# Performance work log

Measured on AMD Instinct MI355X. Metric: run time of the kernel, lower is better.

Reference implementation:

```python
import jax, jax.numpy as jnp
from jax import lax
import numpy as np

SCALE = 3.0
TOPK = 16  # eigvec[:, -16:] in the original module
BN_EPS = 1e-5
DN = ('NCHW', 'OIHW', 'NCHW')


def setup_inputs() -> dict:
    key = jax.random.key(0)
    ks = jax.random.split(key, 8)
    B, C, H, W = 16, 256, 64, 64
    x = jax.random.normal(ks[0], (B, C, H, W), dtype=jnp.float32)
    conv1_w = jax.random.normal(ks[1], (C, C, 1, 1), dtype=jnp.float32) * (1.0 / np.sqrt(C))
    conv1_b = jax.random.normal(ks[2], (C,), dtype=jnp.float32) * 0.01
    conv2_w = jax.random.normal(ks[3], (C, C, 3, 3), dtype=jnp.float32) * (1.0 / np.sqrt(9 * C))
    bn_gamma = jnp.ones((C,), dtype=jnp.float32)
    bn_beta = jnp.zeros((C,), dtype=jnp.float32)
    bn_mean = jax.random.normal(ks[4], (C,), dtype=jnp.float32) * 0.1
    bn_var = jax.random.uniform(ks[5], (C,), dtype=jnp.float32, minval=0.5, maxval=1.5)
    return {"x": x, "conv1_w": conv1_w, "conv1_b": conv1_b, "conv2_w": conv2_w,
            "bn_gamma": bn_gamma, "bn_beta": bn_beta, "bn_mean": bn_mean, "bn_var": bn_var}


def reference(x, conv1_w, conv1_b, conv2_w, bn_gamma, bn_beta, bn_mean, bn_var):
    B, C, H, W = x.shape
    # conv1: 1x1 conv with bias
    gx = lax.conv_general_dilated(x, conv1_w, (1, 1), 'SAME', dimension_numbers=DN)
    gx = gx + conv1_b[None, :, None, None]
    # center over spatial positions: [B, C, N]
    g = gx.reshape(B, C, H * W)
    g = g - jnp.mean(g, axis=-1, keepdims=True)
    # per-batch covariance, divided by batch size (faithful to original gx.shape[0])
    cmat = jnp.einsum('bcn,bdn->bcd', g, g) / B  # [B, C, C]
    # batched symmetric eigendecomposition (ascending eigenvalues, like torch.symeig)
    _, vecs = jnp.linalg.eigh(cmat)              # vecs: [B, C, C]
    w = jnp.swapaxes(vecs[..., -TOPK:], -1, -2)  # top-16 eigvecs, [B, 16, C]
    # project onto eigvec subspace, softmax over the 16 components (dim=1)
    z = jax.nn.softmax(jnp.einsum('bkc,bcn->bkn', w, g) * SCALE, axis=1)  # [B, 16, N]
    y = jnp.einsum('bkc,bkn->bcn', w, z).reshape(B, C, H, W)
    # conv2: 3x3 conv (no bias) + BatchNorm (eval mode with running stats)
    att = lax.conv_general_dilated(y, conv2_w, (1, 1), 'SAME', dimension_numbers=DN)
    inv = bn_gamma * lax.rsqrt(bn_var + BN_EPS)
    att = att * inv[None, :, None, None] + (bn_beta - bn_mean * inv)[None, :, None, None]
    return x + att
```

## Files before the change

### kernel.cpp

```cpp
#include <hip/hip_runtime.h>
#include <hip/hip_bf16.h>
#include <math.h>


typedef __hip_bfloat16 bf16;

#define NB 16
#define NC 256
#define NSP 4096
#define LAPACK_EPS32 5.9604644775390625e-08

#define PHB_I0 80
#define PHB_M  176

__device__ __forceinline__ float b2f(bf16 v){ return __bfloat162float(v); }
__device__ __forceinline__ double safelog(double x){
  double a = fabs(x);
  if (!(a > 0.0) || !isfinite(a)) a = 1e-300;
  return log(a);
}

__device__ __forceinline__ float blk_reduce_sum(float s, float* red, int tid){
  red[tid] = s; __syncthreads();
  if (tid < 128) red[tid] += red[tid+128];
  __syncthreads();
  if (tid < 64){
    float x = red[tid] + red[tid+64];
    #pragma unroll
    for (int o = 32; o > 0; o >>= 1) x += __shfl_down(x, o);
    if (tid == 0) red[0] = x;
  }
  __syncthreads();
  return red[0];
}

__device__ __forceinline__ float blk_reduce_sum512(float s, float* red, int tid){
  red[tid] = s; __syncthreads();
  if (tid < 256) red[tid] += red[tid+256];
  __syncthreads();
  if (tid < 128) red[tid] += red[tid+128];
  __syncthreads();
  if (tid < 64){
    float x = red[tid] + red[tid+64];
    #pragma unroll
    for (int o = 32; o > 0; o >>= 1) x += __shfl_down(x, o);
    if (tid == 0) red[0] = x;
  }
  __syncthreads();
  return red[0];
}

__global__ __launch_bounds__(256) void k_detect(const unsigned short* __restrict__ xr,
                                                int* __restrict__ flags){
  __shared__ int red[256];
  int tid = threadIdx.x;
  int cnt = 0;
  for (int i = tid; i < 4096; i += 256){
    unsigned int u = xr[i];
    unsigned int e = (u >> 7) & 0xFF;
    if (e >= 134) ++cnt;
  }
  red[tid] = cnt; __syncthreads();
  for (int o=128;o>0;o>>=1){ if(tid<o) red[tid]+=red[tid+o]; __syncthreads(); }
  if (tid==0) flags[0] = (red[0] > 50) ? 1 : 0;
}

__global__ __launch_bounds__(256) void k_conv1(const void* __restrict__ xv_,
                                               const void* __restrict__ w1v,
                                               const int* __restrict__ flags,
                                               float* __restrict__ g){
  __shared__ __attribute__((aligned(16))) float ws[256][16];
  int nt = blockIdx.x, ct = blockIdx.y, b = blockIdx.z;
  int tid = threadIdx.x;
  int c0 = ct*16;
  int isf = flags[0];
  if (isf){
    const float* w1 = (const float*)w1v;
    for (int i = tid; i < 16*256; i += 256)
      ws[i&255][i>>8] = w1[(size_t)(c0 + (i>>8))*256 + (i&255)];
  } else {
    const bf16* w1 = (const bf16*)w1v;
    for (int i = tid; i < 16*256; i += 256)
      ws[i&255][i>>8] = b2f(w1[(size_t)(c0 + (i>>8))*256 + (i&255)]);
  }
  __syncthreads();
  int n = nt*256 + tid;
  float acc[16];
  #pragma unroll
  for (int i=0;i<16;++i) acc[i]=0.f;
  if (isf){
    const float* xp = (const float*)xv_ + (size_t)b*NC*NSP + n;
    for (int d=0; d<256; ++d){
      float xv = xp[(size_t)d*NSP];
      float4 wa=*(const float4*)&ws[d][0];
      float4 wb=*(const float4*)&ws[d][4];
      float4 wc=*(const float4*)&ws[d][8];
      float4 wd=*(const float4*)&ws[d][12];
      acc[0] =fmaf(wa.x,xv,acc[0]);  acc[1] =fmaf(wa.y,xv,acc[1]);
      acc[2] =fmaf(wa.z,xv,acc[2]);  acc[3] =fmaf(wa.w,xv,acc[3]);
      acc[4] =fmaf(wb.x,xv,acc[4]);  acc[5] =fmaf(wb.y,xv,acc[5]);
      acc[6] =fmaf(wb.z,xv,acc[6]);  acc[7] =fmaf(wb.w,xv,acc[7]);
      acc[8] =fmaf(wc.x,xv,acc[8]);  acc[9] =fmaf(wc.y,xv,acc[9]);
      acc[10]=fmaf(wc.z,xv,acc[10]); acc[11]=fmaf(wc.w,xv,acc[11]);
      acc[12]=fmaf(wd.x,xv,acc[12]); acc[13]=fmaf(wd.y,xv,acc[13]);
      acc[14]=fmaf(wd.z,xv,acc[14]); acc[15]=fmaf(wd.w,xv,acc[15]);
    }
  } else {
    const bf16* xp = (const bf16*)xv_ + (size_t)b*NC*NSP + n;
    for (int d=0; d<256; ++d){
      float xv = b2f(xp[(size_t)d*NSP]);
      float4 wa=*(const float4*)&ws[d][0];
      float4 wb=*(const float4*)&ws[d][4];
      float4 wc=*(const float4*)&ws[d][8];
      float4 wd=*(const float4*)&ws[d][12];
      acc[0] =fmaf(wa.x,xv,acc[0]);  acc[1] =fmaf(wa.y,xv,acc[1]);
      acc[2] =fmaf(wa.z,xv,acc[2]);  acc[3] =fmaf(wa.w,xv,acc[3]);
      acc[4] =fmaf(wb.x,xv,acc[4]);  acc[5] =fmaf(wb.y,xv,acc[5]);
      acc[6] =fmaf(wb.z,xv,acc[6]);  acc[7] =fmaf(wb.w,xv,acc[7]);
      acc[8] =fmaf(wc.x,xv,acc[8]);  acc[9] =fmaf(wc.y,xv,acc[9]);
      acc[10]=fmaf(wc.z,xv,acc[10]); acc[11]=fmaf(wc.w,xv,acc[11]);
      acc[12]=fmaf(wd.x,xv,acc[12]); acc[13]=fmaf(wd.y,xv,acc[13]);
      acc[14]=fmaf(wd.z,xv,acc[14]); acc[15]=fmaf(wd.w,xv,acc[15]);
    }
  }
  float* gp = g + ((size_t)b*NC + c0)*NSP + n;
  #pragma unroll
  for (int i=0;i<16;++i) gp[(size_t)i*NSP] = acc[i];
}

__global__ __launch_bounds__(256) void k_center(float* __restrict__ g){
  int bc = blockIdx.x;
  float* p = g + (size_t)bc*NSP;
  int tid = threadIdx.x;
  __shared__ float red[256];
  float s = 0.f;
  for (int i=tid;i<NSP;i+=256) s += p[i];
  red[tid]=s; __syncthreads();
  for (int o=128;o>0;o>>=1){ if(tid<o) red[tid]+=red[tid+o]; __syncthreads(); }
  float mean = red[0] * (1.0f/4096.0f);
  for (int i=tid;i<NSP;i+=256) p[i] -= mean;
}

__global__ __launch_bounds__(256) void k_cmat(const float* __restrict__ g,
                                              float* __restrict__ A){
  __shared__ float t1[32][65];
  __shared__ float t2[32][65];
  int bx = blockIdx.x, by = blockIdx.y, b = blockIdx.z;
  int tid = threadIdx.x;
  int tx = tid & 31, ty = tid >> 5;
  const float* gb = g + (size_t)b*NC*NSP;
  float acc[4] = {0.f,0.f,0.f,0.f};
  for (int ch=0; ch<64; ++ch){
    int n0 = ch*64;
    for (int idx=tid; idx<2048; idx+=256){
      int r = idx>>6, cc = idx&63;
      t1[r][cc] = gb[(size_t)(by*32 + r)*NSP + n0 + cc];
      t2[r][cc] = gb[(size_t)(bx*32 + r)*NSP + n0 + cc];
    }
    __syncthreads();
    for (int kk=0; kk<64; ++kk){
      float v2 = t2[tx][kk];
      #pragma unroll
      for (int jj=0;jj<4;++jj) acc[jj] = fmaf(t1[ty+8*jj][kk], v2, acc[jj]);
    }
    __syncthreads();
  }
  #pragma unroll
  for (int jj=0;jj<4;++jj){
    int row = by*32 + ty + 8*jj, col = bx*32 + tx;
    A[((size_t)b*NC + row)*NC + col] = acc[jj]*(1.0f/16.0f);
  }
}

__global__ __launch_bounds__(512,1) void k_sytd2(float* __restrict__ Ag,
                                                 float* __restrict__ e_g,
                                                 float* __restrict__ tau_g,
                                                 float* __restrict__ d_g){
  int b = blockIdx.x, tid = threadIdx.x;
  int rid = tid & 255, half = tid >> 8;
  float* A = Ag + (size_t)b*65536;
  __shared__ float Asub[PHB_M*PHB_M];
  __shared__ float v[256], wv[256];
  __shared__ float red[512];
  __shared__ float accbuf[512];

  for (int i=0;i<PHB_I0;++i){
    float alpha = A[(size_t)i*256+(i+1)];
    float s=0.f;
    { int r=i+2+tid; if (r<256){ float a=A[(size_t)i*256+r]; s=a*a; } }
    float xnorm2 = blk_reduce_sum512(s, red, tid);
    float tau=0.f, scale=0.f, beta=alpha;
    if (xnorm2 > 0.f){
      float r_ = sqrtf(alpha*alpha + xnorm2);
      beta = (alpha >= 0.f) ? -r_ : r_;
      tau = (beta - alpha)/beta;
      scale = 1.0f/(alpha - beta);
    }
    if (tid==0){ e_g[b*256+i] = beta; tau_g[b*256+i] = tau; }
    if (tau != 0.f){
      { int r=i+1+tid;
        if (r<256){
          float val = (r==i+1)?1.0f : A[(size_t)i*256+r]*scale;
          A[(size_t)i*256+r] = val;  v[r] = val;
        }
      }
      __syncthreads();
      int r = i+1+rid;
      bool rv = (r < 256);
      int cmid = (i+1+256) >> 1;
      int cstart = (half==0)? (i+1) : cmid;
      int cend   = (half==0)? cmid  : 256;
      {
        float acc=0.f;
        if (rv){
          const float* Ar = A + r;
          int nfull = (cend-cstart) >> 4;
          float b0[16], b1[16];
          if (nfull>0){
            #pragma unroll
            for (int u=0;u<16;++u) b0[u] = Ar[(size_t)(cstart+u)*256];
          }
          int t=0;
          for (; t+2<=nfull; t+=2){
            int cB = cstart+(t+1)*16;
            #pragma unroll
            for (int u=0;u<16;++u) b1[u] = Ar[(size_t)(cB+u)*256];
            int cA = cstart+t*16;
            #pragma unroll
            for (int u=0;u<16;++u) acc = fmaf(b0[u], v[cA+u], acc);
            if (t+2 < nfull){
              int cC = cstart+(t+2)*16;
              #pragma unroll
              for (int u=0;u<16;++u) b0[u] = Ar[(size_t)(cC+u)*256];
            }
            #pragma unroll
            for (int u=0;u<16;++u) acc = fmaf(b1[u], v[cB+u], acc);
          }
          if (t<nfull){
            int cA = cstart+t*16;
            #pragma unroll
            for (int u=0;u<16;++u) acc = fmaf(b0[u], v[cA+u], acc);
            ++t;
          }
          for (int c2=cstart+nfull*16; c2<cend; ++c2)
            acc = fmaf(Ar[(size_t)c2*256], v[c2], acc);
        }
        accbuf[half*256+rid] = acc;
      }
      __syncthreads();
      if (half==0 && rv) wv[r] = tau*(accbuf[rid] + accbuf[256+rid]);
      __syncthreads();
      float sd = (half==0 && rv)? v[r]*wv[r] : 0.f;
      float dotv = blk_reduce_sum512(sd, red, tid);
      float a2 = -0.5f*tau*dotv;
      if (half==0 && rv) wv[r] += a2*v[r];
      __syncthreads();
      if (rv){
        float vr=v[r], wr=wv[r];
        float* Arw = A + r;
        int nfull = (cend-cstart) >> 4;
        float b0[16], b1[16];
        if (nfull>0){
          #pragma unroll
          for (int u=0;u<16;++u) b0[u] = Arw[(size_t)(cstart+u)*256];
        }
        int t=0;
        for (; t+2<=nfull; t+=2){
          int cB = cstart+(t+1)*16;
          #pragma unroll
          for (int u=0;u<16;++u) b1[u] = Arw[(size_t)(cB+u)*256];
          int cA = cstart+t*16;
          #pragma unroll
          for (int u=0;u<16;++u) b0[u] -= vr*wv[cA+u] + wr*v[cA+u];
          #pragma unroll
          for (int u=0;u<16;++u) Arw[(size_t)(cA+u)*256] = b0[u];
          if (t+2 < nfull){
            int cC = cstart+(t+2)*16;
            #pragma unroll
            for (int u=0;u<16;++u) b0[u] = Arw[(size_t)(cC+u)*256];
          }
          #pragma unroll
          for (int u=0;u<16;++u) b1[u] -= vr*wv[cB+u] + wr*v[cB+u];
          #pragma unroll
          for (int u=0;u<16;++u) Arw[(size_t)(cB+u)*256] = b1[u];
        }
        if (t<nfull){
          int cA = cstart+t*16;
          #pragma unroll
          for (int u=0;u<16;++u) b0[u] -= vr*wv[cA+u] + wr*v[cA+u];
          #pragma unroll
          for (int u=0;u<16;++u) Arw[(size_t)(cA+u)*256] = b0[u];
          ++t;
        }
        for (int c2=cstart+nfull*16; c2<cend; ++c2)
          Arw[(size_t)c2*256] -= vr*wv[c2] + wr*v[c2];
      }
      __syncthreads();
    }
    __syncthreads();
  }

  for (int idx=tid; idx<PHB_M*PHB_M; idx+=512){
    int cc = idx / PHB_M, rr = idx - cc*PHB_M;
    Asub[idx] = A[(size_t)(PHB_I0+cc)*256 + (PHB_I0+rr)];
  }
  __syncthreads();

  for (int i=PHB_I0;i<255;++i){
    int cb = (i - PHB_I0)*PHB_M;
    float alpha = Asub[cb + (i+1-PHB_I0)];
    float s=0.f;
    { int r=i+2+tid; if (r<256){ float a=Asub[cb + (r-PHB_I0)]; s=a*a; } }
    float xnorm2 = blk_reduce_sum512(s, red, tid);
    float tau=0.f, scale=0.f, beta=alpha;
    if (xnorm2 > 0.f){
      float r_ = sqrtf(alpha*alpha + xnorm2);
      beta = (alpha >= 0.f) ? -r_ : r_;
      tau = (beta - alpha)/beta;
      scale = 1.0f/(alpha - beta);
    }
    if (tid==0){ e_g[b*256+i] = beta; tau_g[b*256+i] = tau; }
    if (tau != 0.f){
      { int r=i+1+tid;
        if (r<256){
          float val = (r==i+1)?1.0f : Asub[cb+(r-PHB_I0)]*scale;
          Asub[cb+(r-PHB_I0)] = val;
          A[(size_t)i*256+r] = val;
          v[r] = val;
        }
      }
      __syncthreads();
      int r = i+1+rid;
      bool rv = (r < 256);
      int ro = r - PHB_I0;
      int cmid = (i+1+256) >> 1;
      int cstart = (half==0)? (i+1) : cmid;
      int cend   = (half==0)? cmid  : 256;
      {
        float acc=0.f;
        if (rv){
          int nfull = (cend-cstart) >> 4;
          for (int t=0;t<nfull;++t){
            int cA = cstart + t*16;
            float av[16];
            #pragma unroll
            for (int u=0;u<16;++u) av[u] = Asub[(cA+u-PHB_I0)*PHB_M + ro];
            #pragma unroll
            for (int u=0;u<16;++u) acc = fmaf(av[u], v[cA+u], acc);
          }
          for (int c2=cstart+nfull*16;c2<cend;++c2)
            acc = fmaf(Asub[(c2-PHB_I0)*PHB_M+ro], v[c2], acc);
        }
        accbuf[half*256+rid] = acc;
      }
      __syncthreads();
      if (half==0 && rv) wv[r] = tau*(accbuf[rid] + accbuf[256+rid]);
      __syncthreads();
      float sd = (half==0 && rv)? v[r]*wv[r] : 0.f;
      float dotv = blk_reduce_sum512(sd, red, tid);
      float a2 = -0.5f*tau*dotv;
      if (half==0 && rv) wv[r] += a2*v[r];
      __syncthreads();
      if (rv){
        float vr=v[r], wr=wv[r];
        int nfull = (cend-cstart) >> 4;
        for (int t=0;t<nfull;++t){
          int cA=cstart+t*16;
          float av[16];
          #pragma unroll
          for (int u=0;u<16;++u) av[u] = Asub[(cA+u-PHB_I0)*PHB_M+ro];
          #pragma unroll
          for (int u=0;u<16;++u) av[u] -= vr*wv[cA+u] + wr*v[cA+u];
          #pragma unroll
          for (int u=0;u<16;++u) Asub[(cA+u-PHB_I0)*PHB_M+ro] = av[u];
        }
        for (int c2=cstart+nfull*16;c2<cend;++c2)
          Asub[(c2-PHB_I0)*PHB_M+ro] -= vr*wv[c2] + wr*v[c2];
      }
      __syncthreads();
    }
    __syncthreads();
  }
  if (tid < 256){
    int r = tid;
    float dv = (r >= PHB_I0)? Asub[(r-PHB_I0)*PHB_M + (r-PHB_I0)] : A[(size_t)r*256+r];
    d_g[b*256+r] = dv;
  }
}

__global__ __launch_bounds__(256) void k_leaf(const float* __restrict__ d_g,
                                              const float* __restrict__ e_g,
                                              float* __restrict__ Qg,
                                              double* __restrict__ Dw_g,
                                              double* __restrict__ emod_g){
  int b = blockIdx.x, tid = threadIdx.x;
  float* Q = Qg + (size_t)b*65536;
  double* Dw = Dw_g + (size_t)b*256;
  __shared__ double As[16*257];
  __shared__ float  Vt[16*257];
  __shared__ double dms[256];
  __shared__ double emod[256];
  __shared__ float redf[256];

  float dv = d_g[b*256+tid];
  float ev = (tid<255)? e_g[b*256+tid] : 0.f;
  redf[tid] = fmaxf(fabsf(dv), fabsf(ev)); __syncthreads();
  for(int o=128;o>0;o>>=1){ if(tid<o) redf[tid]=fmaxf(redf[tid],redf[tid+o]); __syncthreads(); }
  double sigma = (double)redf[0];
  if (!(sigma > 0.0)) sigma = 1.0;
  double dmod = (double)dv;
  if ((tid & 15)==15 && tid<255) dmod -= fabs((double)e_g[b*256+tid]);
  if ((tid & 15)==0  && tid>0)   dmod -= fabs((double)e_g[b*256+tid-1]);
  dmod /= sigma;
  double em = (tid<255)? ((double)ev)/sigma : 0.0;
  dms[tid] = dmod;  emod[tid] = em;
  emod_g[b*256+tid] = em;
  __syncthreads();

  int l16 = tid & ~15, j = tid & 15;
  for (int r=0;r<16;++r){
    double av = 0.0;
    if (r==j)        av = dms[l16+j];
    else if (r==j-1) av = emod[l16+j-1];
    else if (r==j+1) av = emod[l16+j];
    As[r*257+tid] = av;
    Vt[r*257+tid] = (r==j)? 1.f : 0.f;
  }
  __syncthreads();

  for (int sweep=0; sweep<14; ++sweep){
    for (int p=0;p<15;++p){
      for (int q=p+1;q<16;++q){
        double app = As[p*257 + l16+p];
        double aqq = As[q*257 + l16+q];
        double apq = As[p*257 + l16+q];
        bool rot = (fabs(apq) > 1e-18);
        double c, s;
        if (rot){
          double theta = (aqq - app)/(2.0*apq);
          double t = 1.0/(fabs(theta)+sqrt(1.0+theta*theta));
          if (theta < 0.0) t = -t;
          c = 1.0/sqrt(1.0+t*t); s = t*c;
        } else { c = 1.0; s = 0.0; }
        double apj = As[p*257 + tid];
        double aqj = As[q*257 + tid];
        double npj = c*apj - s*aqj;
        double nqj = s*apj + c*aqj;
        if (rot && j==p){ npj = c*c*app - 2.0*c*s*apq + s*s*aqq; nqj = 0.0; }
        if (rot && j==q){ npj = 0.0; nqj = s*s*app + 2.0*c*s*apq + c*c*aqq; }
        As[p*257 + tid] = npj;
        As[q*257 + tid] = nqj;
        As[j*257 + l16+p] = npj;
        As[j*257 + l16+q] = nqj;
        float vp = Vt[p*257 + tid], vq = Vt[q*257 + tid];
        Vt[p*257 + tid] = (float)(c*(double)vp - s*(double)vq);
        Vt[q*257 + tid] = (float)(s*(double)vp + c*(double)vq);
      }
    }
  }
  __syncthreads();
  double myval = As[j*257 + l16+j];
  int rank = 0;
  for (int k=0;k<16;++k){
    double vk = As[k*257 + l16+k];
    if (vk < myval || (vk==myval && k<j)) ++rank;
  }
  Dw[l16+rank] = myval;
  for (int r=0;r<16;++r)
    Q[(size_t)(l16+r)*256 + (l16+rank)] = Vt[j*257 + l16+r];
}

struct DCMerge {
  double z_[256], dsv[256], ds2[256], zs2[256];
  double dl_[256], zl_[256], taus[256], ztil[256], normk[256], evo[256];
  double rotcs[256][2];
  int    cs2[256], colx[256], non_[256], defl_[256], anch[256], osrc[256], otyp[256];
  int    roti[256][2];
};

__global__ __launch_bounds__(256) void k_msolve(int lev,
                                                const double* __restrict__ emod_g,
                                                float* __restrict__ Qsrc,
                                                double* __restrict__ Dw_g,
                                                double* __restrict__ Sdl,
                                                double* __restrict__ Sztil,
                                                double* __restrict__ Staus,
                                                double* __restrict__ Snk,
                                                int* __restrict__ Scolx,
                                                int* __restrict__ Sanch,
                                                int* __restrict__ Sotyp,
                                                int* __restrict__ Sosrc,
                                                int* __restrict__ SK){
  int mrg = blockIdx.x, b = blockIdx.y, tid = threadIdx.x;
  float* Q  = Qsrc + (size_t)b*65536;
  double* Dw = Dw_g + (size_t)b*256;
  int slot = b*8 + mrg;
  __shared__ DCMerge mg;
  __shared__ int bci[4];

  int ssz = 16<<lev, nm = ssz<<1;
  int base = mrg*nm;
  double rho0 = emod_g[b*256 + base+ssz-1];
  if (tid < nm){
    float zf = (tid < ssz) ? Q[(size_t)(base+ssz-1)*256 + base + tid]
                           : Q[(size_t)(base+ssz)*256   + base + tid];
    double zz = (double)zf;
    if (rho0 < 0.0 && tid >= ssz) zz = -zz;
    mg.z_[tid] = zz * 0.70710678118654752440;
    mg.dsv[tid] = Dw[base+tid];
  }
  __syncthreads();
  double rho = fabs(2.0*rho0);
  if (tid==0){
    int i1=0, i2=ssz, o=0;
    while (i1<ssz || i2<nm){
      bool take1;
      if (i1>=ssz) take1=false; else if (i2>=nm) take1=true;
      else take1 = (mg.dsv[i1] <= mg.dsv[i2]);
      int src = take1? i1++ : i2++;
      mg.ds2[o]=mg.dsv[src]; mg.zs2[o]=mg.z_[src]; mg.cs2[o]=src; ++o;
    }
  }
  __syncthreads();
  mg.taus[tid] = (tid<nm)? fabs(mg.zs2[tid]) : 0.0; __syncthreads();
  for(int o2=128;o2>0;o2>>=1){ if(tid<o2) mg.taus[tid]=fmax(mg.taus[tid],mg.taus[tid+o2]); __syncthreads(); }
  double zmax = mg.taus[0]; __syncthreads();
  mg.taus[tid] = (tid<nm)? fabs(mg.ds2[tid]) : 0.0; __syncthreads();
  for(int o2=128;o2>0;o2>>=1){ if(tid<o2) mg.taus[tid]=fmax(mg.taus[tid],mg.taus[tid+o2]); __syncthreads(); }
  double dmax = mg.taus[0]; __syncthreads();
  double tol = 8.0*LAPACK_EPS32*fmax(dmax, zmax);
  if (tid==0){
    int K=0, nd=0, nrot=0, pj=-1;
    for (int j=0;j<nm;++j){
      if (rho*fabs(mg.zs2[j]) <= tol){ mg.defl_[nd++]=j; continue; }
      if (pj>=0){
        double sg=mg.zs2[pj], cg=mg.zs2[j];
        double tg=mg.ds2[j]-mg.ds2[pj];
        double taug=sqrt(cg*cg+sg*sg);
        double cn, sn;
        if (taug > 0.0){ cn=cg/taug; sn=-sg/taug; } else { cn=1.0; sn=0.0; }
        if (fabs(tg*cn*sn) <= tol){
          mg.zs2[j]=taug; mg.zs2[pj]=0.0;
          mg.roti[nrot][0]=mg.cs2[pj]; mg.roti[nrot][1]=mg.cs2[j];
          mg.rotcs[nrot][0]=cn; mg.rotcs[nrot][1]=sn; ++nrot;
          double t2 = mg.ds2[pj]*cn*cn + mg.ds2[j]*sn*sn;
          mg.ds2[j] = mg.ds2[pj]*sn*sn + mg.ds2[j]*cn*cn;
          mg.ds2[pj] = t2;
          mg.defl_[nd++]=pj;
          pj=j;
        } else { mg.non_[K++]=pj; pj=j; }
      } else pj=j;
    }
    if (pj>=0) mg.non_[K++]=pj;
    bci[0]=K; bci[1]=nd; bci[2]=nrot;
  }
  __syncthreads();
  int K=bci[0], nd=bci[1], nrot=bci[2];
  for (int r2=0;r2<nrot;++r2){
    int ca = base + mg.roti[r2][0], cb2 = base + mg.roti[r2][1];
    double cn = mg.rotcs[r2][0], sn = mg.rotcs[r2][1];
    if (tid < nm){
      int row = base+tid;
      float xv = Q[(size_t)row*256+ca], yv = Q[(size_t)row*256+cb2];
      Q[(size_t)row*256+ca]  = (float)(cn*(double)xv + sn*(double)yv);
      Q[(size_t)row*256+cb2] = (float)(cn*(double)yv - sn*(double)xv);
    }
    __syncthreads();
  }
  if (tid<K){
    mg.dl_[tid]=mg.ds2[mg.non_[tid]];
    mg.zl_[tid]=mg.zs2[mg.non_[tid]];
    mg.colx[tid]=mg.cs2[mg.non_[tid]];
  }
  __syncthreads();
  mg.taus[tid] = (tid<K)? mg.zl_[tid]*mg.zl_[tid] : 0.0; __syncthreads();
  for(int o2=128;o2>0;o2>>=1){ if(tid<o2) mg.taus[tid]+=mg.taus[tid+o2]; __syncthreads(); }
  double zsum2 = mg.taus[0]; __syncthreads();
  if (tid<K){
    int j=tid;
    double left=mg.dl_[j];
    double right=(j<K-1)? mg.dl_[j+1] : (mg.dl_[K-1] + rho*zsum2);
    double mid=0.5*(left+right);
    double fm=1.0;
    for (int i3=0;i3<K;++i3){
      double del=mg.dl_[i3]-mid;
      fm += rho*mg.zl_[i3]*mg.zl_[i3]/del;
    }
    int a; double lo, hi;
    if (j==K-1){
      a=K-1;
      if (fm<=0.0){ lo=mid-left; hi=right-left; } else { lo=0.0; hi=mid-left; }
    } else if (fm<=0.0){ a=j+1; lo=mid-mg.dl_[j+1]; hi=0.0; }
    else { a=j; lo=0.0; hi=mid-left; }
    double da2=mg.dl_[a];
    double t;
    if (hi > lo){
      t=0.5*(lo+hi);
    } else {
      t = (a==j)? 1e-300 : -1e-300;
      lo = fmin(lo, t); hi = fmax(hi, t);
    }
    for (int it=0; it<100; ++it){
      double gg=1.0, dg=0.0;
      for (int i3=0;i3<K;++i3){
        double del=(mg.dl_[i3]-da2)-t;
        double q=mg.zl_[i3]/del;
        gg += rho*mg.zl_[i3]*q;
        dg += rho*q*q;
      }
      if (gg<0.0) lo=t; else hi=t;
      double tn = t - gg/dg;
      if (!isfinite(tn) || !(tn>lo && tn<hi)) tn=0.5*(lo+hi);
      if (tn == 0.0) tn = (t!=0.0)? t*0.5 : ((a==j)?1e-300:-1e-300);
      double dstep=fabs(tn-t);
      t=tn;
      if (dstep <= 1e-15*(fabs(t)+1e-30)) break;
      if ((hi-lo) <= 1e-15*(fabs(da2)+fabs(t)+1e-30)) break;
    }
    if (t == 0.0 || !isfinite(t)) t = (a==j)? 1e-300 : -1e-300;
    mg.taus[j]=t; mg.anch[j]=a;
  }
  __syncthreads();
  if (tid<K){
    int i3=tid; double acc=0.0; double di=mg.dl_[i3];
    for (int j=0;j<K;++j){
      double lmd = (mg.dl_[mg.anch[j]] - di) + mg.taus[j];
      acc += safelog(lmd);
      if (j!=i3) acc -= safelog(mg.dl_[j]-di);
    }
    double mag = exp(0.5*acc);
    if (!isfinite(mag)) mag = 0.0;
    mg.ztil[i3] = (mg.zl_[i3] >= 0.0)? mag : -mag;
  }
  __syncthreads();
  if (tid<K){
    int j=tid; double da2=mg.dl_[mg.anch[j]]; double tj=mg.taus[j];
    double nr=0.0;
    for (int i3=0;i3<K;++i3){
      double del=(mg.dl_[i3]-da2)-tj;
      if (del == 0.0) del = (tj>=0.0)? -1e-300 : 1e-300;
      double sv=mg.ztil[i3]/del;
      nr += sv*sv;
    }
    if (!(nr > 0.0) || !isfinite(nr)) nr = 1.0;
    mg.normk[j]=sqrt(nr);
  }
  __syncthreads();
  if (tid==0){
    for (int a2=1;a2<nd;++a2){
      int key=mg.defl_[a2]; double kv=mg.ds2[key]; int b2=a2-1;
      while (b2>=0 && mg.ds2[mg.defl_[b2]] > kv){ mg.defl_[b2+1]=mg.defl_[b2]; --b2; }
      mg.defl_[b2+1]=key;
    }
    int i1=0,i2=0,o=0;
    while (i1<K || i2<nd){
      double v1 = (i1<K)? (mg.dl_[mg.anch[i1]]+mg.taus[i1]) : 0.0;
      double v2 = (i2<nd)? mg.ds2[mg.defl_[i2]] : 0.0;
      bool take1;
      if (i1>=K) take1=false; else if (i2>=nd) take1=true; else take1 = (v1 <= v2);
      if (take1){ mg.otyp[o]=0; mg.osrc[o]=i1; mg.evo[o]=v1; ++i1; }
      else { mg.otyp[o]=1; mg.osrc[o]=mg.cs2[mg.defl_[i2]]; mg.evo[o]=v2; ++i2; }
      ++o;
    }
  }
  __syncthreads();
  if (tid<nm) Dw[base+tid]=mg.evo[tid];
  size_t so = (size_t)slot*256;
  if (tid<K){
    Sdl[so+tid]=mg.dl_[tid]; Sztil[so+tid]=mg.ztil[tid];
    Staus[so+tid]=mg.taus[tid]; Snk[so+tid]=mg.normk[tid];
    Scolx[so+tid]=mg.colx[tid]; Sanch[so+tid]=mg.anch[tid];
  }
  if (tid<nm){ Sotyp[so+tid]=mg.otyp[tid]; Sosrc[so+tid]=mg.osrc[tid]; }
  if (tid==0) SK[slot]=K;
}

__global__ __launch_bounds__(256) void k_mvec(int lev,
                                              const float* __restrict__ Qsrc_g,
                                              float* __restrict__ Qdst_g,
                                              const double* __restrict__ Sdl,
                                              const double* __restrict__ Sztil,
                                              const double* __restrict__ Staus,
                                              const double* __restrict__ Snk,
                                              const int* __restrict__ Scolx,
                                              const int* __restrict__ Sanch,
                                              const int* __restrict__ Sotyp,
                                              const int* __restrict__ Sosrc,
                                              const int* __restrict__ SK){
  int t = blockIdx.x, mrg = blockIdx.y, b = blockIdx.z, tid = threadIdx.x;
  const float* Q = Qsrc_g + (size_t)b*65536;
  float* Qd = Qdst_g + (size_t)b*65536;
  int slot = b*8 + mrg;
  size_t so = (size_t)slot*256;
  int ssz = 16<<lev, nm = ssz<<1;
  int base = mrg*nm;
  int p0 = t*16;
  int K = SK[slot];

  __shared__ float svf[256*16];
  __shared__ double cda[16], ctj[16];
  __shared__ float cnk[16];
  __shared__ int ctyp[16], csrc[16];

  if (tid < 16){
    int p = p0 + tid;
    int typ = Sotyp[so+p], src = Sosrc[so+p];
    ctyp[tid]=typ; csrc[tid]=src;
    if (typ==0){
      int j = src;
      cda[tid] = Sdl[so + Sanch[so+j] - 0 + 0];
    }
  }
  __syncthreads();
  if (tid < 16){
    int p = p0 + tid;
    if (ctyp[tid]==0){
      int j = csrc[tid];
      int a = Sanch[so+j];
      cda[tid] = Sdl[so+a];
      ctj[tid] = Staus[so+j];
      cnk[tid] = (float)Snk[so+j];
    } else { cda[tid]=0.0; ctj[tid]=1.0; cnk[tid]=1.f; }
  }
  __syncthreads();
  for (int idx = tid; idx < K*16; idx += 256){
    int i3 = idx >> 4, c = idx & 15;
    float sv = 0.f;
    if (ctyp[c]==0){
      double del = (Sdl[so+i3] - cda[c]) - ctj[c];
      if (del == 0.0) del = (ctj[c]>=0.0)? -1e-300 : 1e-300;
      sv = (float)( Sztil[so+i3]/del / (double)cnk[c] );
      if (!isfinite(sv)) sv = 0.f;
    }
    svf[i3*16 + c] = sv;
  }
  __syncthreads();

  if (tid < nm){
    int row = base + tid;
    const float* Qr = Q + (size_t)row*256 + base;
    float acc[16];
    #pragma unroll
    for (int c=0;c<16;++c) acc[c]=0.f;
    for (int i3=0;i3<K;++i3){
      float qv = Qr[Scolx[so+i3]];
      #pragma unroll
      for (int c=0;c<16;++c) acc[c] = fmaf(qv, svf[i3*16+c], acc[c]);
    }
    #pragma unroll
    for (int c=0;c<16;++c){
      float v = acc[c];
      if (ctyp[c]==1) v = Qr[csrc[c]];
      if (!isfinite(v)) v = 0.f;
      Qd[(size_t)row*256 + base + p0 + c] = v;
    }
  }
}

__global__ __launch_bounds__(512,1) void k_backtf(const float* __restrict__ Ag,
                                                  const float* __restrict__ tau_g,
                                                  const float* __restrict__ Qg,
                                                  float* __restrict__ w16g){
  int b=blockIdx.x, tid=threadIdx.x;
  const float* A=Ag+(size_t)b*65536;
  const float* Q=Qg+(size_t)b*65536;
  __shared__ float U[256][17];
  __shared__ float pd[32][17];
  __shared__ float dk[16];
  int k=tid&15, rg=tid>>4;
  for (int r=rg;r<256;r+=32) U[r][k]=Q[(size_t)r*256+240+k];
  __syncthreads();
  for (int i=254;i>=0;--i){
    float tau=tau_g[b*256+i];
    if (tau!=0.f){
      int r0 = i+1+rg;
      float ar[8];
      #pragma unroll
      for (int u=0;u<8;++u){
        int r = r0 + u*32;
        ar[u] = (r<256)? A[(size_t)i*256+r] : 0.f;
      }
      float uv[8];
      #pragma unroll
      for (int u=0;u<8;++u){
        int r = r0 + u*32;
        uv[u] = (r<256)? U[r][k] : 0.f;
      }
      float s=0.f;
      #pragma unroll
      for (int u=0;u<8;++u){
        int r = r0 + u*32;
        if (r<256) s += ar[u]*uv[u];
      }
      pd[rg][k]=s;
      __syncthreads();
      if (tid<16){
        float acc=0.f;
        #pragma unroll
        for (int gg=0; gg<32; ++gg) acc+=pd[gg][tid];
        dk[tid]=tau*acc;
      }
      __syncthreads();
      float dkk = dk[k];
      #pragma unroll
      for (int u=0;u<8;++u){
        int r = r0 + u*32;
        if (r<256) U[r][k] -= dkk*ar[u];
      }
      __syncthreads();
    }
  }
  for (int c2=rg;c2<256;c2+=32){
    float uv = U[c2][k];
    if (!isfinite(uv)) uv = 0.f;
    w16g[((size_t)b*16+k)*256+c2]=uv;
  }
}

__global__ __launch_bounds__(256) void k_score(const float* __restrict__ g,
                                               const float* __restrict__ w16,
                                               float* __restrict__ z){
  __shared__ __attribute__((aligned(16))) float ws[256][16];
  int nt=blockIdx.x, b=blockIdx.y, tid=threadIdx.x;
  for (int i=tid;i<4096;i+=256) ws[i&255][i>>8]=w16[(size_t)b*4096+i];
  __syncthreads();
  int n=nt*256+tid;
  const float* gp=g+(size_t)b*NC*NSP+n;
  float acc[16];
  #pragma unroll
  for(int k2=0;k2<16;++k2) acc[k2]=0.f;
  for (int c2=0;c2<256;++c2){
    float gv=gp[(size_t)c2*NSP];
    float4 wa=*(const float4*)&ws[c2][0];
    float4 wb=*(const float4*)&ws[c2][4];
    float4 wc=*(const float4*)&ws[c2][8];
    float4 wd=*(const float4*)&ws[c2][12];
    acc[0] =fmaf(wa.x,gv,acc[0]);  acc[1] =fmaf(wa.y,gv,acc[1]);
    acc[2] =fmaf(wa.z,gv,acc[2]);  acc[3] =fmaf(wa.w,gv,acc[3]);
    acc[4] =fmaf(wb.x,gv,acc[4]);  acc[5] =fmaf(wb.y,gv,acc[5]);
    acc[6] =fmaf(wb.z,gv,acc[6]);  acc[7] =fmaf(wb.w,gv,acc[7]);
    acc[8] =fmaf(wc.x,gv,acc[8]);  acc[9] =fmaf(wc.y,gv,acc[9]);
    acc[10]=fmaf(wc.z,gv,acc[10]); acc[11]=fmaf(wc.w,gv,acc[11]);
    acc[12]=fmaf(wd.x,gv,acc[12]); acc[13]=fmaf(wd.y,gv,acc[13]);
    acc[14]=fmaf(wd.z,gv,acc[14]); acc[15]=fmaf(wd.w,gv,acc[15]);
  }
  float mx=-1e30f;
  #pragma unroll
  for(int k2=0;k2<16;++k2){ acc[k2]*=3.0f; mx=fmaxf(mx,acc[k2]); }
  float sum=0.f;
  #pragma unroll
  for(int k2=0;k2<16;++k2){ acc[k2]=expf(acc[k2]-mx); sum+=acc[k2]; }
  float inv=1.0f/sum;
  float* zp=z+(size_t)b*16*NSP+n;
  #pragma unroll
  for(int k2=0;k2<16;++k2) zp[(size_t)k2*NSP]=acc[k2]*inv;
}

__global__ __launch_bounds__(256) void k_y(const float* __restrict__ z,
                                           const float* __restrict__ w16,
                                           float* __restrict__ y){
  __shared__ __attribute__((aligned(16))) float ws[256][16];
  int nt=blockIdx.x, b=blockIdx.y, tid=threadIdx.x;
  for (int i=tid;i<4096;i+=256) ws[i&255][i>>8]=w16[(size_t)b*4096+i];
  __syncthreads();
  int n=nt*256+tid;
  const float* zp=z+(size_t)b*16*NSP+n;
  float zr[16];
  #pragma unroll
  for(int k2=0;k2<16;++k2) zr[k2]=zp[(size_t)k2*NSP];
  float* yp=y+(size_t)b*NC*NSP+n;
  for (int c2=0;c2<256;++c2){
    float4 wa=*(const float4*)&ws[c2][0];
    float4 wb=*(const float4*)&ws[c2][4];
    float4 wc=*(const float4*)&ws[c2][8];
    float4 wd=*(const float4*)&ws[c2][12];
    float acc=0.f;
    acc=fmaf(wa.x,zr[0],acc);  acc=fmaf(wa.y,zr[1],acc);
    acc=fmaf(wa.z,zr[2],acc);  acc=fmaf(wa.w,zr[3],acc);
    acc=fmaf(wb.x,zr[4],acc);  acc=fmaf(wb.y,zr[5],acc);
    acc=fmaf(wb.z,zr[6],acc);  acc=fmaf(wb.w,zr[7],acc);
    acc=fmaf(wc.x,zr[8],acc);  acc=fmaf(wc.y,zr[9],acc);
    acc=fmaf(wc.z,zr[10],acc); acc=fmaf(wc.w,zr[11],acc);
    acc=fmaf(wd.x,zr[12],acc); acc=fmaf(wd.y,zr[13],acc);
    acc=fmaf(wd.z,zr[14],acc); acc=fmaf(wd.w,zr[15],acc);
    yp[(size_t)c2*NSP]=acc;
  }
}

__global__ __launch_bounds__(256) void k_conv2(const float* __restrict__ y,
                                               const void* __restrict__ w2v,
                                               const void* __restrict__ xv_,
                                               const void* __restrict__ gmv,
                                               const void* __restrict__ btv,
                                               const void* __restrict__ muv,
                                               const void* __restrict__ vrv,
                                               const int* __restrict__ flags,
                                               void* __restrict__ outv){
  __shared__ float yt[8][6][66];
  __shared__ float wt[16][8][9];
  int ht=blockIdx.x, ct=blockIdx.y, b=blockIdx.z, tid=threadIdx.x;
  int hl=tid>>6, wl=tid&63;
  int h=ht*4+hl;
  int c0=ct*16;
  int isf = flags[0];
  float acc[16];
  #pragma unroll
  for(int i=0;i<16;++i) acc[i]=0.f;
  const float* yb = y + (size_t)b*NC*NSP;
  for (int d0=0; d0<256; d0+=8){
    for (int idx=tid; idx<8*6*64; idx+=256){
      int dd=idx/384; int rem=idx-dd*384; int rr=rem>>6; int cc2=rem&63;
      int hg=ht*4-1+rr;
      float v = (hg>=0 && hg<64)? yb[(size_t)(d0+dd)*NSP + hg*64 + cc2] : 0.f;
      yt[dd][rr][cc2+1]=v;
    }
    if (tid<48){ int dd=tid/6, rr=tid-dd*6; yt[dd][rr][0]=0.f; yt[dd][rr][65]=0.f; }
    if (isf){
      const float* w2 = (const float*)w2v;
      for (int idx=tid; idx<16*8*9; idx+=256){
        int cc=idx/72; int rem=idx-cc*72; int dd=rem/9; int kk=rem-dd*9;
        wt[cc][dd][kk]=w2[ ((size_t)(c0+cc)*256 + d0+dd)*9 + kk ];
      }
    } else {
      const bf16* w2 = (const bf16*)w2v;
      for (int idx=tid; idx<16*8*9; idx+=256){
        int cc=idx/72; int rem=idx-cc*72; int dd=rem/9; int kk=rem-dd*9;
        wt[cc][dd][kk]=b2f(w2[ ((size_t)(c0+cc)*256 + d0+dd)*9 + kk ]);
      }
    }
    __syncthreads();
    for (int cc=0; cc<16; ++cc){
      float a=acc[cc];
      #pragma unroll
      for (int dd=0; dd<8; ++dd){
        const float* wp=wt[cc][dd];
        a = fmaf(wp[0], yt[dd][hl+0][wl+0], a);
        a = fmaf(wp[1], yt[dd][hl+0][wl+1], a);
        a = fmaf(wp[2], yt[dd][hl+0][wl+2], a);
        a = fmaf(wp[3], yt[dd][hl+1][wl+0], a);
        a = fmaf(wp[4], yt[dd][hl+1][wl+1], a);
        a = fmaf(wp[5], yt[dd][hl+1][wl+2], a);
        a = fmaf(wp[6], yt[dd][hl+2][wl+0], a);
        a = fmaf(wp[7], yt[dd][hl+2][wl+1], a);
        a = fmaf(wp[8], yt[dd][hl+2][wl+2], a);
      }
      acc[cc]=a;
    }
    __syncthreads();
  }
  size_t nidx=(size_t)h*64+wl;
  for (int cc=0;cc<16;++cc){
    int c=c0+cc;
    float gmf, btf, muf, vrf, xvv;
    size_t oi = ((size_t)b*NC+c)*NSP + nidx;
    if (isf){
      gmf=((const float*)gmv)[c]; btf=((const float*)btv)[c];
      muf=((const float*)muv)[c]; vrf=((const float*)vrv)[c];
      xvv=((const float*)xv_)[oi];
    } else {
      gmf=b2f(((const bf16*)gmv)[c]); btf=b2f(((const bf16*)btv)[c]);
      muf=b2f(((const bf16*)muv)[c]); vrf=b2f(((const bf16*)vrv)[c]);
      xvv=b2f(((const bf16*)xv_)[oi]);
    }
    float inv = gmf * rsqrtf(vrf + 1e-5f);
    float shift = btf - muf*inv;
    float val = xvv + acc[cc]*inv + shift;
    if (isf) ((float*)outv)[oi] = val;
    else     ((bf16*)outv)[oi] = __float2bfloat16(val);
  }
}

extern "C" void kernel_launch(void* const* d_in, const int* in_sizes, int n_in,
                              void* d_out, int out_size, void* d_ws, size_t ws_size,
                              hipStream_t stream) {
  const void* x   = d_in[0];
  const void* w1  = d_in[1];
  const void* w2  = d_in[3];
  const void* gmm = d_in[4];
  const void* bet = d_in[5];
  const void* mu  = d_in[6];
  const void* var = d_in[7];

  float* g    = (float*)d_ws;
  float* A    = g   + (size_t)NB*NC*NSP;
  float* Qa   = A   + (size_t)NB*NC*NC;
  float* Qb   = Qa  + (size_t)NB*NC*NC;
  float* w16  = Qb  + (size_t)NB*NC*NC;
  float* zb   = w16 + (size_t)NB*16*NC;
  float* e_g  = zb  + (size_t)NB*16*NSP;
  float* tau_g= e_g + (size_t)NB*NC;
  float* d_g  = tau_g + (size_t)NB*NC;
  double* Dw  = (double*)(d_g + (size_t)NB*NC);
  double* emod_g = Dw + (size_t)NB*NC;
  double* Sdl   = emod_g + (size_t)NB*NC;
  double* Sztil = Sdl   + (size_t)128*256;
  double* Staus = Sztil + (size_t)128*256;
  double* Snk   = Staus + (size_t)128*256;
  int* Scolx = (int*)(Snk + (size_t)128*256);
  int* Sanch = Scolx + (size_t)128*256;
  int* Sotyp = Sanch + (size_t)128*256;
  int* Sosrc = Sotyp + (size_t)128*256;
  int* SK    = Sosrc + (size_t)128*256;
  int* flags = SK + 256;
  size_t needed = (size_t)((char*)(flags + 16) - (char*)d_ws);
  if (ws_size < needed) return;

  hipMemsetAsync(Qa, 0, (size_t)NB*NC*NC*2*sizeof(float), stream);
  k_detect<<<dim3(1),256,0,stream>>>((const unsigned short*)x, flags);
  k_conv1 <<<dim3(16,16,16),256,0,stream>>>(x, w1, flags, g);
  k_center<<<dim3(NB*NC),256,0,stream>>>(g);
  k_cmat  <<<dim3(8,8,16),256,0,stream>>>(g, A);
  k_sytd2 <<<dim3(16),512,0,stream>>>(A, e_g, tau_g, d_g);
  k_leaf  <<<dim3(16),256,0,stream>>>(d_g, e_g, Qa, Dw, emod_g);
  k_msolve<<<dim3(8,16),256,0,stream>>>(0, emod_g, Qa, Dw, Sdl,Sztil,Staus,Snk,Scolx,Sanch,Sotyp,Sosrc,SK);
  k_mvec  <<<dim3(2,8,16),256,0,stream>>>(0, Qa, Qb, Sdl,Sztil,Staus,Snk,Scolx,Sanch,Sotyp,Sosrc,SK);
  k_msolve<<<dim3(4,16),256,0,stream>>>(1, emod_g, Qb, Dw, Sdl,Sztil,Staus,Snk,Scolx,Sanch,Sotyp,Sosrc,SK);
  k_mvec  <<<dim3(4,4,16),256,0,stream>>>(1, Qb, Qa, Sdl,Sztil,Staus,Snk,Scolx,Sanch,Sotyp,Sosrc,SK);
  k_msolve<<<dim3(2,16),256,0,stream>>>(2, emod_g, Qa, Dw, Sdl,Sztil,Staus,Snk,Scolx,Sanch,Sotyp,Sosrc,SK);
  k_mvec  <<<dim3(8,2,16),256,0,stream>>>(2, Qa, Qb, Sdl,Sztil,Staus,Snk,Scolx,Sanch,Sotyp,Sosrc,SK);
  k_msolve<<<dim3(1,16),256,0,stream>>>(3, emod_g, Qb, Dw, Sdl,Sztil,Staus,Snk,Scolx,Sanch,Sotyp,Sosrc,SK);
  k_mvec  <<<dim3(16,1,16),256,0,stream>>>(3, Qb, Qa, Sdl,Sztil,Staus,Snk,Scolx,Sanch,Sotyp,Sosrc,SK);
  k_backtf<<<dim3(16),512,0,stream>>>(A, tau_g, Qa, w16);
  k_score <<<dim3(16,16),256,0,stream>>>(g, w16, zb);
  k_y     <<<dim3(16,16),256,0,stream>>>(zb, w16, g);
  k_conv2 <<<dim3(16,16,16),256,0,stream>>>(g, w2, x, gmm, bet, mu, var, flags, d_out);
}
```

Measured before the change: 7.483 ms.

## Fuse score/softmax with back-projection and enlarge conv2 spatial tile per thread

Merges the projection+softmax kernel with the y reconstruction kernel, so each thread keeps its 16 softmax weights in registers and writes y in place over g. This drops the z intermediate buffer and one launch. The 3x3 conv2 kernel now covers 8 rows per block, with each thread computing two output columns. That halves the grid and cuts the halo overhead on the shared y tile, at the cost of more registers per thread.

```diff
diff --git a/kernel.cpp b/kernel.cpp
--- a/kernel.cpp
+++ b/kernel.cpp
@@ -817,15 +817,14 @@
   }
 }
 
-__global__ __launch_bounds__(256) void k_score(const float* __restrict__ g,
-                                               const float* __restrict__ w16,
-                                               float* __restrict__ z){
+__global__ __launch_bounds__(256) void k_scy(float* __restrict__ g,
+                                             const float* __restrict__ w16){
   __shared__ __attribute__((aligned(16))) float ws[256][16];
   int nt=blockIdx.x, b=blockIdx.y, tid=threadIdx.x;
   for (int i=tid;i<4096;i+=256) ws[i&255][i>>8]=w16[(size_t)b*4096+i];
   __syncthreads();
   int n=nt*256+tid;
-  const float* gp=g+(size_t)b*NC*NSP+n;
+  float* gp=g+(size_t)b*NC*NSP+n;
   float acc[16];
   #pragma unroll
   for(int k2=0;k2<16;++k2) acc[k2]=0.f;
@@ -851,39 +850,23 @@
   #pragma unroll
   for(int k2=0;k2<16;++k2){ acc[k2]=expf(acc[k2]-mx); sum+=acc[k2]; }
   float inv=1.0f/sum;
-  float* zp=z+(size_t)b*16*NSP+n;
   #pragma unroll
-  for(int k2=0;k2<16;++k2) zp[(size_t)k2*NSP]=acc[k2]*inv;
-}
-
-__global__ __launch_bounds__(256) void k_y(const float* __restrict__ z,
-                                           const float* __restrict__ w16,
-                                           float* __restrict__ y){
-  __shared__ __attribute__((aligned(16))) float ws[256][16];
-  int nt=blockIdx.x, b=blockIdx.y, tid=threadIdx.x;
-  for (int i=tid;i<4096;i+=256) ws[i&255][i>>8]=w16[(size_t)b*4096+i];
-  __syncthreads();
-  int n=nt*256+tid;
-  const float* zp=z+(size_t)b*16*NSP+n;
-  float zr[16];
-  #pragma unroll
-  for(int k2=0;k2<16;++k2) zr[k2]=zp[(size_t)k2*NSP];
-  float* yp=y+(size_t)b*NC*NSP+n;
+  for(int k2=0;k2<16;++k2) acc[k2]*=inv;
   for (int c2=0;c2<256;++c2){
     float4 wa=*(const float4*)&ws[c2][0];
     float4 wb=*(const float4*)&ws[c2][4];
     float4 wc=*(const float4*)&ws[c2][8];
     float4 wd=*(const float4*)&ws[c2][12];
-    float acc=0.f;
-    acc=fmaf(wa.x,zr[0],acc);  acc=fmaf(wa.y,zr[1],acc);
-    acc=fmaf(wa.z,zr[2],acc);  acc=fmaf(wa.w,zr[3],acc);
-    acc=fmaf(wb.x,zr[4],acc);  acc=fmaf(wb.y,zr[5],acc);
-    acc=fmaf(wb.z,zr[6],acc);  acc=fmaf(wb.w,zr[7],acc);
-    acc=fmaf(wc.x,zr[8],acc);  acc=fmaf(wc.y,zr[9],acc);
-    acc=fmaf(wc.z,zr[10],acc); acc=fmaf(wc.w,zr[11],acc);
-    acc=fmaf(wd.x,zr[12],acc); acc=fmaf(wd.y,zr[13],acc);
-    acc=fmaf(wd.z,zr[14],acc); acc=fmaf(wd.w,zr[15],acc);
-    yp[(size_t)c2*NSP]=acc;
+    float a=0.f;
+    a=fmaf(wa.x,acc[0],a);  a=fmaf(wa.y,acc[1],a);
+    a=fmaf(wa.z,acc[2],a);  a=fmaf(wa.w,acc[3],a);
+    a=fmaf(wb.x,acc[4],a);  a=fmaf(wb.y,acc[5],a);
+    a=fmaf(wb.z,acc[6],a);  a=fmaf(wb.w,acc[7],a);
+    a=fmaf(wc.x,acc[8],a);  a=fmaf(wc.y,acc[9],a);
+    a=fmaf(wc.z,acc[10],a); a=fmaf(wc.w,acc[11],a);
+    a=fmaf(wd.x,acc[12],a); a=fmaf(wd.y,acc[13],a);
+    a=fmaf(wd.z,acc[14],a); a=fmaf(wd.w,acc[15],a);
+    gp[(size_t)c2*NSP]=a;
   }
 }
 
@@ -896,25 +879,25 @@
                                                const void* __restrict__ vrv,
                                                const int* __restrict__ flags,
                                                void* __restrict__ outv){
-  __shared__ float yt[8][6][66];
+  __shared__ float yt[8][10][66];
   __shared__ float wt[16][8][9];
   int ht=blockIdx.x, ct=blockIdx.y, b=blockIdx.z, tid=threadIdx.x;
-  int hl=tid>>6, wl=tid&63;
-  int h=ht*4+hl;
+  int wl=tid&31, hl=tid>>5;
+  int h=ht*8+hl;
   int c0=ct*16;
   int isf = flags[0];
-  float acc[16];
+  float accA[16], accB[16];
   #pragma unroll
-  for(int i=0;i<16;++i) acc[i]=0.f;
+  for(int i=0;i<16;++i){ accA[i]=0.f; accB[i]=0.f; }
   const float* yb = y + (size_t)b*NC*NSP;
   for (int d0=0; d0<256; d0+=8){
-    for (int idx=tid; idx<8*6*64; idx+=256){
-      int dd=idx/384; int rem=idx-dd*384; int rr=rem>>6; int cc2=rem&63;
-      int hg=ht*4-1+rr;
+    for (int idx=tid; idx<8*10*64; idx+=256){
+      int dd=idx/640; int rem=idx-dd*640; int rr=rem>>6; int cc2=rem&63;
+      int hg=ht*8-1+rr;
       float v = (hg>=0 && hg<64)? yb[(size_t)(d0+dd)*NSP + hg*64 + cc2] : 0.f;
       yt[dd][rr][cc2+1]=v;
     }
-    if (tid<48){ int dd=tid/6, rr=tid-dd*6; yt[dd][rr][0]=0.f; yt[dd][rr][65]=0.f; }
+    if (tid<80){ int dd=tid/10, rr=tid-dd*10; yt[dd][rr][0]=0.f; yt[dd][rr][65]=0.f; }
     if (isf){
       const float* w2 = (const float*)w2v;
       for (int idx=tid; idx<16*8*9; idx+=256){
@@ -930,7 +913,7 @@
     }
     __syncthreads();
     for (int cc=0; cc<16; ++cc){
-      float a=acc[cc];
+      float a=accA[cc], c=accB[cc];
       #pragma unroll
       for (int dd=0; dd<8; ++dd){
         const float* wp=wt[cc][dd];
@@ -943,30 +926,43 @@
         a = fmaf(wp[6], yt[dd][hl+2][wl+0], a);
         a = fmaf(wp[7], yt[dd][hl+2][wl+1], a);
         a = fmaf(wp[8], yt[dd][hl+2][wl+2], a);
-      }
-      acc[cc]=a;
+        c = fmaf(wp[0], yt[dd][hl+0][wl+32], c);
+        c = fmaf(wp[1], yt[dd][hl+0][wl+33], c);
+        c = fmaf(wp[2], yt[dd][hl+0][wl+34], c);
+        c = fmaf(wp[3], yt[dd][hl+1][wl+32], c);
+        c = fmaf(wp[4], yt[dd][hl+1][wl+33], c);
+        c = fmaf(wp[5], yt[dd][hl+1][wl+34], c);
+        c = fmaf(wp[6], yt[dd][hl+2][wl+32], c);
+        c = fmaf(wp[7], yt[dd][hl+2][wl+33], c);
+        c = fmaf(wp[8], yt[dd][hl+2][wl+34], c);
+      }
+      accA[cc]=a; accB[cc]=c;
     }
     __syncthreads();
   }
-  size_t nidx=(size_t)h*64+wl;
+  size_t n0=(size_t)h*64+wl;
+  size_t n1=n0+32;
   for (int cc=0;cc<16;++cc){
     int c=c0+cc;
-    float gmf, btf, muf, vrf, xvv;
-    size_t oi = ((size_t)b*NC+c)*NSP + nidx;
+    float gmf, btf, muf, vrf, xv0, xv1;
+    size_t oi0 = ((size_t)b*NC+c)*NSP + n0;
+    size_t oi1 = ((size_t)b*NC+c)*NSP + n1;
     if (isf){
       gmf=((const float*)gmv)[c]; btf=((const float*)btv)[c];
       muf=((const float*)muv)[c]; vrf=((const float*)vrv)[c];
-      xvv=((const float*)xv_)[oi];
+      xv0=((const float*)xv_)[oi0]; xv1=((const float*)xv_)[oi1];
     } else {
       gmf=b2f(((const bf16*)gmv)[c]); btf=b2f(((const bf16*)btv)[c]);
       muf=b2f(((const bf16*)muv)[c]); vrf=b2f(((const bf16*)vrv)[c]);
-      xvv=b2f(((const bf16*)xv_)[oi]);
+      xv0=b2f(((const bf16*)xv_)[oi0]); xv1=b2f(((const bf16*)xv_)[oi1]);
     }
     float inv = gmf * rsqrtf(vrf + 1e-5f);
     float shift = btf - muf*inv;
-    float val = xvv + acc[cc]*inv + shift;
-    if (isf) ((float*)outv)[oi] = val;
-    else     ((bf16*)outv)[oi] = __float2bfloat16(val);
+    float v0 = xv0 + accA[cc]*inv + shift;
+    float v1 = xv1 + accB[cc]*inv + shift;
+    if (isf){ ((float*)outv)[oi0] = v0; ((float*)outv)[oi1] = v1; }
+    else    { ((bf16*)outv)[oi0] = __float2bfloat16(v0);
+              ((bf16*)outv)[oi1] = __float2bfloat16(v1); }
   }
 }
 
@@ -1021,7 +1017,6 @@
   k_msolve<<<dim3(1,16),256,0,stream>>>(3, emod_g, Qb, Dw, Sdl,Sztil,Staus,Snk,Scolx,Sanch,Sotyp,Sosrc,SK);
   k_mvec  <<<dim3(16,1,16),256,0,stream>>>(3, Qb, Qa, Sdl,Sztil,Staus,Snk,Scolx,Sanch,Sotyp,Sosrc,SK);
   k_backtf<<<dim3(16),512,0,stream>>>(A, tau_g, Qa, w16);
-  k_score <<<dim3(16,16),256,0,stream>>>(g, w16, zb);
-  k_y     <<<dim3(16,16),256,0,stream>>>(zb, w16, g);
-  k_conv2 <<<dim3(16,16,16),256,0,stream>>>(g, w2, x, gmm, bet, mu, var, flags, d_out);
-}
+  k_scy   <<<dim3(16,16),256,0,stream>>>(g, w16);
+  k_conv2 <<<dim3(8,16,16),256,0,stream>>>(g, w2, x, gmm, bet, mu, var, flags, d_out);
+}
```

Result: slower. 9.411 ms (+25.8%).
